# Kernel optimization log

Measured on AMD Instinct MI355X. Metric: run time of the kernel, lower is better.

## Reference

```python
import jax, jax.numpy as jnp
import numpy as np

B, S, D = 4, 2048, 1024
P = 9            # num_paths
DM = D // 4      # bottleneck d_mid
EPS = 1e-5


def setup_inputs() -> dict:
    key = jax.random.key(0)
    ks = jax.random.split(key, 12)
    sc_in = 1.0 / np.sqrt(D)
    sc_mid = 1.0 / np.sqrt(DM)
    return {
        "x": jax.random.normal(ks[0], (B, S, D), dtype=jnp.float32),
        # neighbor mixer: per-channel 3-tap kernel over the sequence axis
        "mix_kernel": jax.random.normal(ks[1], (3, D), dtype=jnp.float32) * 0.5,
        # 9 parallel bottleneck paths: D -> D/4 -> D
        "W1": jax.random.normal(ks[2], (P, D, DM), dtype=jnp.float32) * sc_in,
        "b1": jnp.zeros((P, DM), dtype=jnp.float32),
        "W2": jax.random.normal(ks[3], (P, DM, D), dtype=jnp.float32) * sc_mid,
        "b2": jnp.zeros((P, D), dtype=jnp.float32),
        # observer: D -> D/4 -> tanh -> ... -> P scores
        "Wo1": jax.random.normal(ks[4], (D, DM), dtype=jnp.float32) * sc_in,
        "bo1": jnp.zeros((DM,), dtype=jnp.float32),
        "Wo2": jax.random.normal(ks[5], (DM, P), dtype=jnp.float32) * sc_mid,
        "bo2": jnp.zeros((P,), dtype=jnp.float32),
        # output norm affine params
        "gamma": jnp.ones((D,), dtype=jnp.float32),
        "beta": jnp.zeros((D,), dtype=jnp.float32),
    }


def _mix(x, mix_kernel):
    # eidosNeighborMixer: local 3-tap depthwise mix along sequence (non-causal)
    xp = jnp.pad(x, ((0, 0), (1, 1), (0, 0)))
    return (mix_kernel[0] * xp[:, :-2]
            + mix_kernel[1] * xp[:, 1:-1]
            + mix_kernel[2] * xp[:, 2:])


def _layernorm(h, gamma, beta):
    mu = jnp.mean(h, axis=-1, keepdims=True)
    var = jnp.var(h, axis=-1, keepdims=True)
    return (h - mu) * jax.lax.rsqrt(var + EPS) * gamma + beta


def reference(x, mix_kernel, W1, b1, W2, b2, Wo1, bo1, Wo2, bo2, gamma, beta):
    x_mixed = _mix(x, mix_kernel)                                   # [B,S,D]
    # all num_paths bottleneck transforms computed densely (as in source)
    h = jnp.einsum("bsd,pdm->bspm", x_mixed, W1) + b1               # [B,S,P,DM]
    stacked_paths = jnp.einsum("bspm,pmd->bspd", h, W2) + b2        # [B,S,P,D]
    # observer scores
    scores = jnp.tanh(x_mixed @ Wo1 + bo1) @ Wo2 + bo2              # [B,S,P]
    # eval-mode collapse: hard argmax one-hot selection
    idx = jnp.argmax(scores, axis=-1)                               # [B,S]
    weights = jax.nn.one_hot(idx, P, dtype=stacked_paths.dtype)     # [B,S,P]
    collapsed = jnp.einsum("bspd,bsp->bsd", stacked_paths, weights)  # [B,S,D]
    return _layernorm(x + collapsed, gamma, beta)
```

## Files before the change

kernel.cpp:

```cpp
#include <hip/hip_runtime.h>
#include <math.h>

#define Ss 2048
#define Dd 1024
#define Pp 9
#define DMm 256
#define Tt 8192
#define EPSf 1e-5f
#define BAND 6e-3f

typedef __attribute__((ext_vector_type(8))) __bf16 bf16x8;
typedef __attribute__((ext_vector_type(4))) float f32x4;

#define GLOBAL_AS __attribute__((address_space(1)))
#define LDS_AS __attribute__((address_space(3)))

#define MAXTILES 137
#define MAXT32   265

__device__ __forceinline__ unsigned short bf16rn(float f) {
  unsigned int u = __float_as_uint(f);
  unsigned int r = (u + 0x7fffu + ((u >> 16) & 1u)) >> 16;
  return (unsigned short)r;
}

__device__ __forceinline__ void gload16(const void* g, void* l) {
  __builtin_amdgcn_global_load_lds((const GLOBAL_AS unsigned int*)g,
                                   (LDS_AS unsigned int*)l, 16, 0, 0);
}

__device__ __forceinline__ int xcd_swz(int bx, int nwg) {
  const int q = nwg >> 3, r = nwg & 7;
  const int xcd = bx & 7, loc = bx >> 3;
  return (xcd < r ? xcd * (q + 1) : r * (q + 1) + (xcd - r) * q) + loc;
}

#define KSW(r, sl) (((r) << 6) + ((((sl) ^ ((r) & 7))) << 3))

__global__ __launch_bounds__(256) void k_prep(const float* __restrict__ x,
    const float* __restrict__ mk, unsigned short* __restrict__ xh,
    const float* __restrict__ W1, const float* __restrict__ W2,
    const float* __restrict__ Wo1,
    unsigned short* __restrict__ W1t, unsigned short* __restrict__ W2t,
    unsigned short* __restrict__ Wo1t, int* __restrict__ counts) {
  const int bid = blockIdx.x;
  if (bid < Tt) {
    if (bid == 0 && threadIdx.x < 64) counts[threadIdx.x] = 0;
    const int t = xcd_swz(bid, Tt);
    const int s = t & (Ss - 1);
    const int d = threadIdx.x << 2;
    const float* xc = x + (size_t)t * Dd + d;
    float4 vb = *(const float4*)xc;
    float4 va = make_float4(0.f, 0.f, 0.f, 0.f);
    float4 vc = make_float4(0.f, 0.f, 0.f, 0.f);
    if (s > 0)      va = *(const float4*)(xc - Dd);
    if (s < Ss - 1) vc = *(const float4*)(xc + Dd);
    const float4 k0 = *(const float4*)(mk + d);
    const float4 k1 = *(const float4*)(mk + Dd + d);
    const float4 k2 = *(const float4*)(mk + 2 * Dd + d);
    float4 o;
    o.x = k0.x * va.x + k1.x * vb.x + k2.x * vc.x;
    o.y = k0.y * va.y + k1.y * vb.y + k2.y * vc.y;
    o.z = k0.z * va.z + k1.z * vb.z + k2.z * vc.z;
    o.w = k0.w * va.w + k1.w * vb.w + k2.w * vc.w;
    ushort4 h;
    h.x = bf16rn(o.x); h.y = bf16rn(o.y); h.z = bf16rn(o.z); h.w = bf16rn(o.w);
    *(ushort4*)(xh + (size_t)t * Dd + d) = h;
    return;
  }
  const int i = bid - Tt;
  const int z = i >> 8, rem = i & 255;
  const int bx = rem & 31, by = rem >> 5;
  const float* in; unsigned short* outp; int R, C, r0, c0;
  if (z < Pp)          { in = W1;  outp = W1t;  R = Dd;  C = DMm; r0 = bx * 32; c0 = by * 32; }
  else if (z < 2 * Pp) { in = W2;  outp = W2t;  R = DMm; C = Dd;  r0 = by * 32; c0 = bx * 32; }
  else                 { in = Wo1; outp = Wo1t; R = Dd;  C = DMm; r0 = bx * 32; c0 = by * 32; }
  const int zi = (z < Pp) ? z : ((z < 2 * Pp) ? z - Pp : 0);
  const size_t zo = (size_t)zi * R * C;
  __shared__ float tile[32][33];
  const int tr = threadIdx.x >> 3, tc = (threadIdx.x & 7) << 2;
  float4 v = *(const float4*)(in + zo + (size_t)(r0 + tr) * C + c0 + tc);
  tile[tr][tc] = v.x; tile[tr][tc + 1] = v.y; tile[tr][tc + 2] = v.z; tile[tr][tc + 3] = v.w;
  __syncthreads();
  ushort4 h;
  h.x = bf16rn(tile[tc + 0][tr]); h.y = bf16rn(tile[tc + 1][tr]);
  h.z = bf16rn(tile[tc + 2][tr]); h.w = bf16rn(tile[tc + 3][tr]);
  *(ushort4*)(outp + zo + (size_t)(c0 + tr) * R + r0 + tc) = h;
}

__global__ __launch_bounds__(256) void k_obs(
    const unsigned short* __restrict__ A,
    const unsigned short* __restrict__ Bt,
    const float* __restrict__ bo1,
    const float* __restrict__ Wo2,
    float* __restrict__ pscore) {
  const int ti = xcd_swz(blockIdx.x, gridDim.x);
  const int tile0 = ti * 32;
  const int n0 = blockIdx.y * 128;
  __shared__ __align__(16) unsigned short As[2][32 * 64];
  __shared__ __align__(16) unsigned short Bs[2][128 * 64];
  __shared__ float sW[128 * Pp];
  __shared__ float part[2][32][Pp];
  const int tid = threadIdx.x;
  for (int l = tid; l < 128 * Pp; l += 256) sW[l] = Wo2[n0 * Pp + l];
  __syncthreads();
  const int w = tid >> 6, lane = tid & 63;
  const int fr = lane & 15, fs = lane >> 4;
  const int wr = w >> 1, wc = w & 1;
  const unsigned short* srcA;
  { const int r = tid >> 3, sl = (tid & 7) ^ (r & 7);
    srcA = A + (size_t)(tile0 + r) * Dd + sl * 8; }
  const unsigned short* srcB[4];
  #pragma unroll
  for (int i = 0; i < 4; ++i) {
    const int u = i * 256 + tid, r = u >> 3, sl = (u & 7) ^ (r & 7);
    srcB[i] = Bt + (size_t)(n0 + r) * Dd + sl * 8;
  }
  const int ldsW = w * 512;
  int aoff[2], boff[4][2];
  #pragma unroll
  for (int kk = 0; kk < 2; ++kk) aoff[kk] = KSW(wr * 16 + fr, kk * 4 + fs);
  #pragma unroll
  for (int n = 0; n < 4; ++n)
    #pragma unroll
    for (int kk = 0; kk < 2; ++kk)
      boff[n][kk] = KSW(wc * 64 + n * 16 + fr, kk * 4 + fs);

#define STAGE(b, kb) do { \
    gload16(srcA + (kb), &As[b][0] + ldsW); \
    gload16(srcB[0] + (kb), &Bs[b][0] + ldsW); \
    gload16(srcB[1] + (kb), &Bs[b][0] + 2048 + ldsW); \
    gload16(srcB[2] + (kb), &Bs[b][0] + 4096 + ldsW); \
    gload16(srcB[3] + (kb), &Bs[b][0] + 6144 + ldsW); \
  } while (0)

  f32x4 acc[4] = {};
  const int NS = Dd / 64;
  STAGE(0, 0);
  for (int s = 0; s < NS; ++s) {
    const int buf = s & 1;
    if (s + 1 < NS) {
      STAGE(buf ^ 1, (s + 1) * 64);
      asm volatile("s_waitcnt vmcnt(5)" ::: "memory");
    } else {
      asm volatile("s_waitcnt vmcnt(0)" ::: "memory");
    }
    __builtin_amdgcn_s_barrier();
    __builtin_amdgcn_sched_barrier(0);
    const unsigned short* Ab = &As[buf][0];
    const unsigned short* Bb_ = &Bs[buf][0];
    bf16x8 a[2], b[4][2];
    #pragma unroll
    for (int kk = 0; kk < 2; ++kk) a[kk] = *(const bf16x8*)&Ab[aoff[kk]];
    #pragma unroll
    for (int n = 0; n < 4; ++n)
      #pragma unroll
      for (int kk = 0; kk < 2; ++kk)
        b[n][kk] = *(const bf16x8*)&Bb_[boff[n][kk]];
    #pragma unroll
    for (int kk = 0; kk < 2; ++kk)
      #pragma unroll
      for (int n = 0; n < 4; ++n)
        acc[n] = __builtin_amdgcn_mfma_f32_16x16x32_bf16(a[kk], b[n][kk], acc[n], 0, 0, 0);
    __builtin_amdgcn_s_barrier();
  }
#undef STAGE

  float ps[4][Pp] = {};
  #pragma unroll
  for (int n = 0; n < 4; ++n) {
    const int cl = wc * 64 + n * 16 + fr;
    const float bv = bo1[n0 + cl];
    #pragma unroll
    for (int j = 0; j < 4; ++j) {
      const float tv = tanhf(acc[n][j] + bv);
      #pragma unroll
      for (int p = 0; p < Pp; ++p) ps[j][p] += tv * sW[cl * Pp + p];
    }
  }
  #pragma unroll
  for (int off = 1; off < 16; off <<= 1)
    #pragma unroll
    for (int j = 0; j < 4; ++j)
      #pragma unroll
      for (int p = 0; p < Pp; ++p)
        ps[j][p] += __shfl_xor(ps[j][p], off);
  if (fr == 0) {
    #pragma unroll
    for (int j = 0; j < 4; ++j)
      #pragma unroll
      for (int p = 0; p < Pp; ++p)
        part[wc][wr * 16 + fs * 4 + j][p] = ps[j][p];
  }
  __syncthreads();
  for (int l = tid; l < 32 * Pp; l += 256) {
    const int r = l / Pp, p = l - r * Pp;
    pscore[(size_t)(tile0 + r) * (2 * Pp) + blockIdx.y * Pp + p] =
        part[0][r][p] + part[1][r][p];
  }
}

__global__ __launch_bounds__(256) void k_amax(const float* __restrict__ pscore,
    const float* __restrict__ bo2,
    int* __restrict__ idx, int* __restrict__ nflag, int* __restrict__ flagged) {
  const int t = blockIdx.x * 256 + threadIdx.x;
  const float* pr = pscore + (size_t)t * (2 * Pp);
  float best = -1e30f, second = -1e30f;
  int bi = 0;
  #pragma unroll
  for (int p = 0; p < Pp; ++p) {
    const float sc = pr[p] + pr[Pp + p] + bo2[p];
    if (sc > best) { second = best; best = sc; bi = p; }
    else if (sc > second) second = sc;
  }
  idx[t] = bi;
  if (best - second < BAND) {
    const int pos = atomicAdd(nflag, 1);
    flagged[pos] = t;
  }
}

template<int KTOT, int NTOT, int MODE, int TM>
__global__ __launch_bounds__(256) void k_gemm(
    const unsigned short* __restrict__ A,
    const unsigned short* __restrict__ Bt,
    const float* __restrict__ bias,
    const float* __restrict__ resid,
    float* __restrict__ outf, unsigned short* __restrict__ outh,
    const int* __restrict__ counts, const int* __restrict__ tokenlist) {
  constexpr int MM = TM / 32;
  int p = 0, ti = xcd_swz(blockIdx.x, gridDim.x), cnt = Tt;
  for (p = 0; p < Pp; ++p) {
    cnt = counts[p];
    const int nt = (cnt + TM - 1) / TM;
    if (ti < nt) break;
    ti -= nt;
  }
  if (p == Pp) return;
  const int tile0 = ti * TM;
  __shared__ int tl[TM];
  __shared__ __align__(16) unsigned short As[2][TM * 64];
  __shared__ __align__(16) unsigned short Bs[2][128 * 64];
  const int tid = threadIdx.x;
  if (tid < TM) {
    const int li = tile0 + tid;
    tl[tid] = (li < cnt) ? tokenlist[p * Tt + li] : tokenlist[p * Tt];
  }
  __syncthreads();
  const int w = tid >> 6, lane = tid & 63;
  const int fr = lane & 15, fs = lane >> 4;
  const int wr = w >> 1, wc = w & 1;
  const int n0 = blockIdx.y * 128;
  const unsigned short* Bp0 = Bt + (size_t)p * NTOT * KTOT + (size_t)n0 * KTOT;
  const unsigned short* srcA[MM];
  #pragma unroll
  for (int i = 0; i < MM; ++i) {
    const int u = i * 256 + tid, r = u >> 3, sl = (u & 7) ^ (r & 7);
    srcA[i] = A + (size_t)tl[r] * KTOT + sl * 8;
  }
  const unsigned short* srcB[4];
  #pragma unroll
  for (int i = 0; i < 4; ++i) {
    const int u = i * 256 + tid, r = u >> 3, sl = (u & 7) ^ (r & 7);
    srcB[i] = Bp0 + (size_t)r * KTOT + sl * 8;
  }
  const int ldsW = w * 512;
  int aoff[MM][2], boff[4][2];
  #pragma unroll
  for (int m = 0; m < MM; ++m)
    #pragma unroll
    for (int kk = 0; kk < 2; ++kk)
      aoff[m][kk] = KSW(wr * (TM / 2) + m * 16 + fr, kk * 4 + fs);
  #pragma unroll
  for (int n = 0; n < 4; ++n)
    #pragma unroll
    for (int kk = 0; kk < 2; ++kk)
      boff[n][kk] = KSW(wc * 64 + n * 16 + fr, kk * 4 + fs);

#define STAGE(b, kb) do { \
    _Pragma("unroll") \
    for (int i = 0; i < MM; ++i) \
      gload16(srcA[i] + (kb), &As[b][0] + i * 2048 + ldsW); \
    gload16(srcB[0] + (kb), &Bs[b][0] + ldsW); \
    gload16(srcB[1] + (kb), &Bs[b][0] + 2048 + ldsW); \
    gload16(srcB[2] + (kb), &Bs[b][0] + 4096 + ldsW); \
    gload16(srcB[3] + (kb), &Bs[b][0] + 6144 + ldsW); \
  } while (0)

  f32x4 acc[MM][4] = {};
  const int NS = KTOT / 64;
  STAGE(0, 0);
  for (int s = 0; s < NS; ++s) {
    const int buf = s & 1;
    if (s + 1 < NS) {
      STAGE(buf ^ 1, (s + 1) * 64);
      if (TM == 64) asm volatile("s_waitcnt vmcnt(6)" ::: "memory");
      else          asm volatile("s_waitcnt vmcnt(5)" ::: "memory");
    } else {
      asm volatile("s_waitcnt vmcnt(0)" ::: "memory");
    }
    __builtin_amdgcn_s_barrier();
    __builtin_amdgcn_sched_barrier(0);
    const unsigned short* Ab = &As[buf][0];
    const unsigned short* Bb_ = &Bs[buf][0];
    bf16x8 a[MM][2], b[4][2];
    #pragma unroll
    for (int m = 0; m < MM; ++m)
      #pragma unroll
      for (int kk = 0; kk < 2; ++kk)
        a[m][kk] = *(const bf16x8*)&Ab[aoff[m][kk]];
    #pragma unroll
    for (int n = 0; n < 4; ++n)
      #pragma unroll
      for (int kk = 0; kk < 2; ++kk)
        b[n][kk] = *(const bf16x8*)&Bb_[boff[n][kk]];
    #pragma unroll
    for (int kk = 0; kk < 2; ++kk)
      #pragma unroll
      for (int m = 0; m < MM; ++m)
        #pragma unroll
        for (int n = 0; n < 4; ++n)
          acc[m][n] = __builtin_amdgcn_mfma_f32_16x16x32_bf16(a[m][kk], b[n][kk], acc[m][n], 0, 0, 0);
    __builtin_amdgcn_s_barrier();
  }
#undef STAGE

  const float* bias_z = bias + (size_t)p * NTOT;
  #pragma unroll
  for (int m = 0; m < MM; ++m) {
    #pragma unroll
    for (int j = 0; j < 4; ++j) {
      const int rr = wr * (TM / 2) + m * 16 + fs * 4 + j;
      const int li = tile0 + rr;
      if (li >= cnt) continue;
      const int t = tl[rr];
      #pragma unroll
      for (int n = 0; n < 4; ++n) {
        const int c = n0 + wc * 64 + n * 16 + fr;
        const float v = acc[m][n][j] + bias_z[c];
        if (MODE == 1) outh[(size_t)t * NTOT + c] = bf16rn(v);
        else           outf[(size_t)t * NTOT + c] = v + resid[(size_t)t * NTOT + c];
      }
    }
  }
}

__global__ __launch_bounds__(256) void k_rescue(const float* __restrict__ x,
    const float* __restrict__ mk,
    const float* __restrict__ Wo1, const float* __restrict__ bo1,
    const float* __restrict__ Wo2, const float* __restrict__ bo2,
    const int* __restrict__ nflag, const int* __restrict__ flagged,
    int* __restrict__ idx) {
  __shared__ double sx[Dd];
  __shared__ double th[DMm];
  __shared__ double red[4][12];
  const int nf = *nflag;
  const int tid = threadIdx.x;
  const int wv = tid >> 6, ln = tid & 63;
  for (int f = blockIdx.x; f < nf; f += gridDim.x) {
    const int t = flagged[f];
    const int s = t & (Ss - 1);
    for (int l = tid; l < Dd; l += 256) {
      const double xa = (s > 0)      ? (double)x[(size_t)(t - 1) * Dd + l] : 0.0;
      const double xb =                (double)x[(size_t)t * Dd + l];
      const double xc = (s < Ss - 1) ? (double)x[(size_t)(t + 1) * Dd + l] : 0.0;
      sx[l] = (double)mk[l] * xa + (double)mk[Dd + l] * xb + (double)mk[2 * Dd + l] * xc;
    }
    __syncthreads();
    {
      double a0 = 0, a1 = 0, a2 = 0, a3 = 0;
      const float* wcol = Wo1 + tid;
      for (int d = 0; d < Dd; d += 4) {
        a0 += sx[d + 0] * (double)wcol[(size_t)(d + 0) * DMm];
        a1 += sx[d + 1] * (double)wcol[(size_t)(d + 1) * DMm];
        a2 += sx[d + 2] * (double)wcol[(size_t)(d + 2) * DMm];
        a3 += sx[d + 3] * (double)wcol[(size_t)(d + 3) * DMm];
      }
      th[tid] = tanh(((a0 + a1) + (a2 + a3)) + (double)bo1[tid]);
    }
    __syncthreads();
    double pr[Pp];
    const double tv = th[tid];
    #pragma unroll
    for (int p = 0; p < Pp; ++p) pr[p] = tv * (double)Wo2[tid * Pp + p];
    #pragma unroll
    for (int off = 32; off > 0; off >>= 1)
      #pragma unroll
      for (int p = 0; p < Pp; ++p) pr[p] += __shfl_xor(pr[p], off);
    if (ln == 0) {
      #pragma unroll
      for (int p = 0; p < Pp; ++p) red[wv][p] = pr[p];
    }
    __syncthreads();
    if (tid == 0) {
      double best = -1e300; int bi = 0;
      #pragma unroll
      for (int p = 0; p < Pp; ++p) {
        const double sv = red[0][p] + red[1][p] + red[2][p] + red[3][p] + (double)bo2[p];
        if (sv > best) { best = sv; bi = p; }
      }
      idx[t] = bi;
    }
    __syncthreads();
  }
}

__global__ __launch_bounds__(256) void k_scatter(const int* __restrict__ idx,
    int* __restrict__ counts, int* __restrict__ tokenlist) {
  __shared__ int lcnt[Pp], lbase[Pp];
  const int tid = threadIdx.x;
  if (tid < Pp) lcnt[tid] = 0;
  __syncthreads();
  const int t = blockIdx.x * 256 + tid;
  const int p = idx[t];
  const int slot = atomicAdd(&lcnt[p], 1);
  __syncthreads();
  if (tid < Pp) lbase[tid] = atomicAdd(&counts[tid], lcnt[tid]);
  __syncthreads();
  tokenlist[p * Tt + lbase[p] + slot] = t;
}

__global__ __launch_bounds__(256) void k_ln(float* __restrict__ y,
    const float* __restrict__ gamma, const float* __restrict__ beta) {
  const int t = blockIdx.x;
  const int d = threadIdx.x << 2;
  float* row = y + (size_t)t * Dd;
  float4 v = *(float4*)(row + d);
  float s = v.x + v.y + v.z + v.w;
  float q = v.x * v.x + v.y * v.y + v.z * v.z + v.w * v.w;
  #pragma unroll
  for (int off = 32; off > 0; off >>= 1) {
    s += __shfl_xor(s, off);
    q += __shfl_xor(q, off);
  }
  __shared__ float ssum[4], sqq[4];
  const int wave = threadIdx.x >> 6, lane = threadIdx.x & 63;
  if (lane == 0) { ssum[wave] = s; sqq[wave] = q; }
  __syncthreads();
  s = ssum[0] + ssum[1] + ssum[2] + ssum[3];
  q = sqq[0] + sqq[1] + sqq[2] + sqq[3];
  const float mu = s * (1.f / Dd);
  const float var = q * (1.f / Dd) - mu * mu;
  const float inv = rsqrtf(var + EPSf);
  const float4 g = *(const float4*)(gamma + d);
  const float4 bt = *(const float4*)(beta + d);
  float4 o;
  o.x = (v.x - mu) * inv * g.x + bt.x;
  o.y = (v.y - mu) * inv * g.y + bt.y;
  o.z = (v.z - mu) * inv * g.z + bt.z;
  o.w = (v.w - mu) * inv * g.w + bt.w;
  *(float4*)(row + d) = o;
}

extern "C" void kernel_launch(void* const* d_in, const int* in_sizes, int n_in,
                              void* d_out, int out_size, void* d_ws, size_t ws_size,
                              hipStream_t stream) {
  (void)in_sizes; (void)n_in; (void)out_size; (void)ws_size;
  const float* x     = (const float*)d_in[0];
  const float* mk    = (const float*)d_in[1];
  const float* W1    = (const float*)d_in[2];
  const float* b1    = (const float*)d_in[3];
  const float* W2    = (const float*)d_in[4];
  const float* b2    = (const float*)d_in[5];
  const float* Wo1   = (const float*)d_in[6];
  const float* bo1   = (const float*)d_in[7];
  const float* Wo2   = (const float*)d_in[8];
  const float* bo2   = (const float*)d_in[9];
  const float* gamma = (const float*)d_in[10];
  const float* beta  = (const float*)d_in[11];
  float* out = (float*)d_out;

  size_t off = 0;
  auto alloc = [&](size_t bytes) -> void* {
    void* p = (char*)d_ws + off;
    off += (bytes + 255) & ~(size_t)255;
    return p;
  };
  unsigned short* xm_h   = (unsigned short*)alloc((size_t)Tt * Dd * 2);
  unsigned short* h1     = (unsigned short*)alloc((size_t)Tt * DMm * 2);
  float*          pscore = (float*)alloc((size_t)Tt * 2 * Pp * 4);
  unsigned short* W1t    = (unsigned short*)alloc((size_t)Pp * Dd * DMm * 2);
  unsigned short* W2t    = (unsigned short*)alloc((size_t)Pp * DMm * Dd * 2);
  unsigned short* Wo1t   = (unsigned short*)alloc((size_t)Dd * DMm * 2);
  int* idx      = (int*)alloc(Tt * 4);
  int* counts   = (int*)alloc(64 * 4);
  int* nflag    = counts + 16;
  int* flagged  = (int*)alloc(Tt * 4);
  int* tokenlist = (int*)alloc((size_t)Pp * Tt * 4);

  k_prep<<<Tt + (2 * Pp + 1) * 256, 256, 0, stream>>>(
      x, mk, xm_h, W1, W2, Wo1, W1t, W2t, Wo1t, counts);

  k_obs<<<dim3(Tt / 32, DMm / 128), 256, 0, stream>>>(
      xm_h, Wo1t, bo1, Wo2, pscore);
  k_amax<<<Tt / 256, 256, 0, stream>>>(pscore, bo2, idx, nflag, flagged);
  k_rescue<<<256, 256, 0, stream>>>(x, mk, Wo1, bo1, Wo2, bo2, nflag, flagged, idx);
  k_scatter<<<Tt / 256, 256, 0, stream>>>(idx, counts, tokenlist);

  k_gemm<Dd, DMm, 1, 32><<<dim3(MAXT32, DMm / 128), 256, 0, stream>>>(
      xm_h, W1t, b1, nullptr, nullptr, h1, counts, tokenlist);
  k_gemm<DMm, Dd, 2, 64><<<dim3(MAXTILES, Dd / 128), 256, 0, stream>>>(
      h1, W2t, b2, x, out, nullptr, counts, tokenlist);
  k_ln<<<Tt, 256, 0, stream>>>(out, gamma, beta);
}
```

Measured before the change: 127.8 us.

## Fuse scatter into argmax and rescue, store pre-norm residual as bf16

Drops the separate scatter kernel and the idx buffer. Confident tokens are appended to per-path token lists directly in the argmax kernel, and ambiguous tokens are appended by the rescue kernel after it recomputes their scores. The second GEMM now writes the residual sum as bf16 into a scratch buffer, which the layernorm reads before writing the fp32 output. This removes one launch and halves the intermediate traffic, at the cost of rounding the pre-norm values to bf16, which could move outputs past tolerance.

```diff
diff --git a/kernel.cpp b/kernel.cpp
--- a/kernel.cpp
+++ b/kernel.cpp
@@ -22,6 +22,10 @@
   unsigned int u = __float_as_uint(f);
   unsigned int r = (u + 0x7fffu + ((u >> 16) & 1u)) >> 16;
   return (unsigned short)r;
+}
+
+__device__ __forceinline__ float b2f(unsigned short h) {
+  return __uint_as_float((unsigned int)h << 16);
 }
 
 __device__ __forceinline__ void gload16(const void* g, void* l) {
@@ -202,8 +206,13 @@
 
 __global__ __launch_bounds__(256) void k_amax(const float* __restrict__ pscore,
     const float* __restrict__ bo2,
-    int* __restrict__ idx, int* __restrict__ nflag, int* __restrict__ flagged) {
-  const int t = blockIdx.x * 256 + threadIdx.x;
+    int* __restrict__ nflag, int* __restrict__ flagged,
+    int* __restrict__ counts, int* __restrict__ tokenlist) {
+  __shared__ int lcnt[Pp], lbase[Pp];
+  const int tid = threadIdx.x;
+  if (tid < Pp) lcnt[tid] = 0;
+  __syncthreads();
+  const int t = blockIdx.x * 256 + tid;
   const float* pr = pscore + (size_t)t * (2 * Pp);
   float best = -1e30f, second = -1e30f;
   int bi = 0;
@@ -213,11 +222,16 @@
     if (sc > best) { second = best; best = sc; bi = p; }
     else if (sc > second) second = sc;
   }
-  idx[t] = bi;
+  int slot = -1;
   if (best - second < BAND) {
-    const int pos = atomicAdd(nflag, 1);
-    flagged[pos] = t;
-  }
+    flagged[atomicAdd(nflag, 1)] = t;
+  } else {
+    slot = atomicAdd(&lcnt[bi], 1);
+  }
+  __syncthreads();
+  if (tid < Pp) lbase[tid] = atomicAdd(&counts[tid], lcnt[tid]);
+  __syncthreads();
+  if (slot >= 0) tokenlist[bi * Tt + lbase[bi] + slot] = t;
 }
 
 template<int KTOT, int NTOT, int MODE, int TM>
@@ -226,7 +240,7 @@
     const unsigned short* __restrict__ Bt,
     const float* __restrict__ bias,
     const float* __restrict__ resid,
-    float* __restrict__ outf, unsigned short* __restrict__ outh,
+    unsigned short* __restrict__ outh,
     const int* __restrict__ counts, const int* __restrict__ tokenlist) {
   constexpr int MM = TM / 32;
   int p = 0, ti = xcd_swz(blockIdx.x, gridDim.x), cnt = Tt;
@@ -337,9 +351,9 @@
       #pragma unroll
       for (int n = 0; n < 4; ++n) {
         const int c = n0 + wc * 64 + n * 16 + fr;
-        const float v = acc[m][n][j] + bias_z[c];
-        if (MODE == 1) outh[(size_t)t * NTOT + c] = bf16rn(v);
-        else           outf[(size_t)t * NTOT + c] = v + resid[(size_t)t * NTOT + c];
+        float v = acc[m][n][j] + bias_z[c];
+        if (MODE == 2) v += resid[(size_t)t * NTOT + c];
+        outh[(size_t)t * NTOT + c] = bf16rn(v);
       }
     }
   }
@@ -350,7 +364,7 @@
     const float* __restrict__ Wo1, const float* __restrict__ bo1,
     const float* __restrict__ Wo2, const float* __restrict__ bo2,
     const int* __restrict__ nflag, const int* __restrict__ flagged,
-    int* __restrict__ idx) {
+    int* __restrict__ counts, int* __restrict__ tokenlist) {
   __shared__ double sx[Dd];
   __shared__ double th[DMm];
   __shared__ double red[4][12];
@@ -399,33 +413,21 @@
         const double sv = red[0][p] + red[1][p] + red[2][p] + red[3][p] + (double)bo2[p];
         if (sv > best) { best = sv; bi = p; }
       }
-      idx[t] = bi;
+      const int pos = atomicAdd(&counts[bi], 1);
+      tokenlist[bi * Tt + pos] = t;
     }
     __syncthreads();
   }
 }
 
-__global__ __launch_bounds__(256) void k_scatter(const int* __restrict__ idx,
-    int* __restrict__ counts, int* __restrict__ tokenlist) {
-  __shared__ int lcnt[Pp], lbase[Pp];
-  const int tid = threadIdx.x;
-  if (tid < Pp) lcnt[tid] = 0;
-  __syncthreads();
-  const int t = blockIdx.x * 256 + tid;
-  const int p = idx[t];
-  const int slot = atomicAdd(&lcnt[p], 1);
-  __syncthreads();
-  if (tid < Pp) lbase[tid] = atomicAdd(&counts[tid], lcnt[tid]);
-  __syncthreads();
-  tokenlist[p * Tt + lbase[p] + slot] = t;
-}
-
-__global__ __launch_bounds__(256) void k_ln(float* __restrict__ y,
+__global__ __launch_bounds__(256) void k_ln(const unsigned short* __restrict__ pre,
+    float* __restrict__ out,
     const float* __restrict__ gamma, const float* __restrict__ beta) {
   const int t = blockIdx.x;
   const int d = threadIdx.x << 2;
-  float* row = y + (size_t)t * Dd;
-  float4 v = *(float4*)(row + d);
+  const ushort4 hv = *(const ushort4*)(pre + (size_t)t * Dd + d);
+  float4 v;
+  v.x = b2f(hv.x); v.y = b2f(hv.y); v.z = b2f(hv.z); v.w = b2f(hv.w);
   float s = v.x + v.y + v.z + v.w;
   float q = v.x * v.x + v.y * v.y + v.z * v.z + v.w * v.w;
   #pragma unroll
@@ -449,7 +451,7 @@
   o.y = (v.y - mu) * inv * g.y + bt.y;
   o.z = (v.z - mu) * inv * g.z + bt.z;
   o.w = (v.w - mu) * inv * g.w + bt.w;
-  *(float4*)(row + d) = o;
+  *(float4*)(out + (size_t)t * Dd + d) = o;
 }
 
 extern "C" void kernel_launch(void* const* d_in, const int* in_sizes, int n_in,
@@ -478,11 +480,11 @@
   };
   unsigned short* xm_h   = (unsigned short*)alloc((size_t)Tt * Dd * 2);
   unsigned short* h1     = (unsigned short*)alloc((size_t)Tt * DMm * 2);
+  unsigned short* pre    = (unsigned short*)alloc((size_t)Tt * Dd * 2);
   float*          pscore = (float*)alloc((size_t)Tt * 2 * Pp * 4);
   unsigned short* W1t    = (unsigned short*)alloc((size_t)Pp * Dd * DMm * 2);
   unsigned short* W2t    = (unsigned short*)alloc((size_t)Pp * DMm * Dd * 2);
   unsigned short* Wo1t   = (unsigned short*)alloc((size_t)Dd * DMm * 2);
-  int* idx      = (int*)alloc(Tt * 4);
   int* counts   = (int*)alloc(64 * 4);
   int* nflag    = counts + 16;
   int* flagged  = (int*)alloc(Tt * 4);
@@ -493,13 +495,14 @@
 
   k_obs<<<dim3(Tt / 32, DMm / 128), 256, 0, stream>>>(
       xm_h, Wo1t, bo1, Wo2, pscore);
-  k_amax<<<Tt / 256, 256, 0, stream>>>(pscore, bo2, idx, nflag, flagged);
-  k_rescue<<<256, 256, 0, stream>>>(x, mk, Wo1, bo1, Wo2, bo2, nflag, flagged, idx);
-  k_scatter<<<Tt / 256, 256, 0, stream>>>(idx, counts, tokenlist);
+  k_amax<<<Tt / 256, 256, 0, stream>>>(pscore, bo2, nflag, flagged,
+                                       counts, tokenlist);
+  k_rescue<<<256, 256, 0, stream>>>(x, mk, Wo1, bo1, Wo2, bo2, nflag, flagged,
+                                    counts, tokenlist);
 
   k_gemm<Dd, DMm, 1, 32><<<dim3(MAXT32, DMm / 128), 256, 0, stream>>>(
-      xm_h, W1t, b1, nullptr, nullptr, h1, counts, tokenlist);
+      xm_h, W1t, b1, nullptr, h1, counts, tokenlist);
   k_gemm<DMm, Dd, 2, 64><<<dim3(MAXTILES, Dd / 128), 256, 0, stream>>>(
-      h1, W2t, b2, x, out, nullptr, counts, tokenlist);
-  k_ln<<<Tt, 256, 0, stream>>>(out, gamma, beta);
-}
+      h1, W2t, b2, x, pre, counts, tokenlist);
+  k_ln<<<Tt, 256, 0, stream>>>(pre, out, gamma, beta);
+}
```

After: 123.5 us (median of 2 runs). -3.4%, faster.
